# Performance work log

Measured on AMD Instinct MI355X. Metric: run time of the kernel, lower is better.

Reference implementation:

```python
import jax, jax.numpy as jnp
import numpy as np

N_NODES = 100000
N_EDGES = 3200000
D_FEAT = 256
HIDDEN = 16
OUT = 256
EPS = 1e-12  # tf.math.l2_normalize epsilon


def setup_inputs() -> dict:
    key = jax.random.key(0)
    ks = jax.random.split(key, 9)
    x = jax.random.normal(ks[0], (N_NODES, D_FEAT), dtype=jnp.float32)
    src = jax.random.randint(ks[1], (N_EDGES,), 0, N_NODES, dtype=jnp.int32)
    dst = jax.random.randint(ks[2], (N_EDGES,), 0, N_NODES, dtype=jnp.int32)
    s_in = 1.0 / np.sqrt(D_FEAT)
    s_h = 1.0 / np.sqrt(HIDDEN)
    W_node = jax.random.normal(ks[3], (D_FEAT, OUT), dtype=jnp.float32) * s_in
    b_node = jnp.zeros((OUT,), dtype=jnp.float32)
    W_agg = jax.random.normal(ks[4], (D_FEAT, HIDDEN), dtype=jnp.float32) * s_in
    b_agg = jnp.zeros((HIDDEN,), dtype=jnp.float32)
    W_neigh = jax.random.normal(ks[5], (HIDDEN, OUT), dtype=jnp.float32) * s_h
    b_neigh = jnp.zeros((OUT,), dtype=jnp.float32)
    return {"x": x, "src": src, "dst": dst,
            "W_node": W_node, "b_node": b_node,
            "W_agg": W_agg, "b_agg": b_agg,
            "W_neigh": W_neigh, "b_neigh": b_neigh}


def reference(x, src, dst, W_node, b_node, W_agg, b_agg, W_neigh, b_neigh):
    # h = node_layer(x)                       [N, OUT]
    h = x @ W_node + b_node
    # agg features on each node = agg_layer(x) [N, HIDDEN]
    h_agg = x @ W_agg + b_agg
    # message = src node's h_agg; reduce = max over incoming edges per dst
    msgs = h_agg[src]                         # [E, HIDDEN]
    agg = jax.ops.segment_max(msgs, dst, num_segments=N_NODES)  # [N, HIDDEN]
    # nodes with no in-edges: DGL zero-fills; segment_max gives -inf
    agg = jnp.where(jnp.isfinite(agg), agg, 0.0)
    # neighs = neighbour_layer(agg)           [N, OUT]
    neighs = agg @ W_neigh + b_neigh
    new_h = jnp.concatenate([h, neighs], axis=-1)  # [N, 2*OUT]
    # activation is identity (None); l2_normalize along last axis
    sq = jnp.sum(new_h * new_h, axis=-1, keepdims=True)
    return new_h * jax.lax.rsqrt(jnp.maximum(sq, EPS))
```

## Files before the change

### kernel.cpp

```cpp
#include <hip/hip_runtime.h>

#define N_NODES 100000
#define N_EDGES 3200000
#define D_FEAT 256
#define HIDDEN 16
#define OUT 256
#define N_TILES 3125
#define PLANE ((size_t)N_NODES * 8)
#define NBUK 196
#define BSZ 512
#define CAP_G 20480
#define NPLANE 4

typedef __attribute__((ext_vector_type(8))) _Float16 half8;
typedef __attribute__((ext_vector_type(4))) float f32x4;

__device__ __forceinline__ unsigned umax32(unsigned a, unsigned b) { return a > b ? a : b; }
__device__ __forceinline__ unsigned pmax16x2(unsigned a, unsigned b) {
    return umax32(a & 0xFFFFu, b & 0xFFFFu) | (umax32(a >> 16, b >> 16) << 16);
}

__device__ __forceinline__ unsigned short enc16(unsigned short u) {
    return (u & 0x8000) ? (unsigned short)~u : (unsigned short)(u | 0x8000);
}
__device__ __forceinline__ _Float16 dec16(unsigned short e) {
    if (e == 0) return (_Float16)0.f;
    unsigned short b = (e & 0x8000) ? (unsigned short)(e & 0x7FFF) : (unsigned short)~e;
    return __builtin_bit_cast(_Float16, b);
}

__device__ __noinline__ void fb_cas(const unsigned* hpk, unsigned* a4, int sv, int dv) {
    #pragma unroll
    for (int p = 0; p < 8; ++p) {
        unsigned mine = hpk[(size_t)sv * 8 + p];
        unsigned* addr = a4 + (size_t)dv * 8 + p;
        unsigned cur = *addr;
        unsigned nv = pmax16x2(cur, mine);
        while (nv != cur) {
            unsigned old = atomicCAS(addr, cur, nv);
            if (old == cur) break;
            cur = old;
            nv = pmax16x2(cur, mine);
        }
    }
}

__global__ void k_pack(const float* __restrict__ Wn, const float* __restrict__ Wng,
                       const float* __restrict__ Wag,
                       _Float16* __restrict__ Wp, _Float16* __restrict__ Wnp,
                       _Float16* __restrict__ Wap)
{
    int id = blockIdx.x * 256 + threadIdx.x;
    if (id < 8192) {
        int l = id & 63, kb = (id >> 6) & 7, nb = id >> 9;
        int col = nb * 16 + (l & 15);
        int k0 = kb * 32 + (l >> 4) * 8;
        half8 v;
        #pragma unroll
        for (int j = 0; j < 8; ++j) v[j] = (_Float16)Wn[(size_t)(k0 + j) * OUT + col];
        ((half8*)Wp)[id] = v;
    } else if (id < 9216) {
        int id2 = id - 8192;
        int l = id2 & 63, nb = id2 >> 6;
        int col = nb * 16 + (l & 15);
        int k0 = (l >> 4) * 8;
        half8 v;
        #pragma unroll
        for (int j = 0; j < 8; ++j) {
            int k = k0 + j;
            v[j] = (k < HIDDEN) ? (_Float16)Wng[(size_t)k * OUT + col] : (_Float16)0.f;
        }
        ((half8*)Wnp)[id2] = v;
    } else if (id < 9728) {
        int id3 = id - 9216;
        int l = id3 & 63, kb = id3 >> 6;
        int col = l & 15;
        int k0 = kb * 32 + (l >> 4) * 8;
        half8 v;
        #pragma unroll
        for (int j = 0; j < 8; ++j) v[j] = (_Float16)Wag[(size_t)(k0 + j) * HIDDEN + col];
        ((half8*)Wap)[id3] = v;
    }
}

__global__ __launch_bounds__(256) void k_gemm(
    const float* __restrict__ x, const _Float16* __restrict__ Wp,
    const _Float16* __restrict__ Wap, const float* __restrict__ b_node,
    const float* __restrict__ b_agg, unsigned* __restrict__ hpk,
    unsigned* __restrict__ aencP, unsigned* __restrict__ gcnt,
    float* __restrict__ out)
{
    __shared__ _Float16 xs[32][256];
    __shared__ unsigned short eagg[32][18];

    int t = threadIdx.x;
    if (blockIdx.x == 0 && t < NBUK) gcnt[t] = 0u;

    int base = blockIdx.x * 32;

    {
        const float4* xg = (const float4*)(x + (size_t)base * D_FEAT) + (size_t)t * 8;
        float4 v[8];
        #pragma unroll
        for (int i = 0; i < 8; ++i) v[i] = xg[i];
        half8* dst = (half8*)(&xs[t >> 3][(t & 7) * 32]);
        #pragma unroll
        for (int i = 0; i < 4; ++i) {
            float4 u0 = v[2 * i], u1 = v[2 * i + 1];
            half8 h;
            h[0]=(_Float16)u0.x; h[1]=(_Float16)u0.y; h[2]=(_Float16)u0.z; h[3]=(_Float16)u0.w;
            h[4]=(_Float16)u1.x; h[5]=(_Float16)u1.y; h[6]=(_Float16)u1.z; h[7]=(_Float16)u1.w;
            dst[i] = h;
        }
    }
    __syncthreads();

    int w = t >> 6, l = t & 63, lr = l & 15, lg = l >> 4;

    f32x4 acc[2][4];
    #pragma unroll
    for (int mb = 0; mb < 2; ++mb)
        #pragma unroll
        for (int nb = 0; nb < 4; ++nb) acc[mb][nb] = (f32x4){0.f, 0.f, 0.f, 0.f};
    f32x4 agga[2];
    #pragma unroll
    for (int mb = 0; mb < 2; ++mb) agga[mb] = (f32x4){0.f, 0.f, 0.f, 0.f};

    const half8* WpV = (const half8*)Wp;
    const half8* WaV = (const half8*)Wap;

    #pragma unroll
    for (int kb = 0; kb < 8; ++kb) {
        half8 a[2];
        #pragma unroll
        for (int mb = 0; mb < 2; ++mb)
            a[mb] = *(const half8*)(&xs[mb * 16 + lr][kb * 32 + lg * 8]);
        half8 b[4];
        #pragma unroll
        for (int nb = 0; nb < 4; ++nb)
            b[nb] = WpV[((w * 4 + nb) * 8 + kb) * 64 + l];
        if (w == 0) {
            half8 bg = WaV[kb * 64 + l];
            #pragma unroll
            for (int mb = 0; mb < 2; ++mb)
                agga[mb] = __builtin_amdgcn_mfma_f32_16x16x32_f16(a[mb], bg, agga[mb], 0, 0, 0);
        }
        #pragma unroll
        for (int mb = 0; mb < 2; ++mb)
            #pragma unroll
            for (int nb = 0; nb < 4; ++nb)
                acc[mb][nb] = __builtin_amdgcn_mfma_f32_16x16x32_f16(
                    a[mb], b[nb], acc[mb][nb], 0, 0, 0);
    }

    if (w == 0) {
        float ba = b_agg[lr];
        #pragma unroll
        for (int mb = 0; mb < 2; ++mb)
            #pragma unroll
            for (int r = 0; r < 4; ++r) {
                float val = agga[mb][r] + ba;
                eagg[mb * 16 + lg * 4 + r][lr] =
                    enc16(__builtin_bit_cast(unsigned short, (_Float16)val));
            }
    }
    __syncthreads();

    {
        int node = t >> 3, p = t & 7;
        int gn = base + node;
        unsigned lo = eagg[node][2 * p], hi = eagg[node][2 * p + 1];
        unsigned word = lo | (hi << 16);
        size_t idx = (size_t)gn * 8 + p;
        hpk[idx] = word;
        aencP[(size_t)NPLANE * PLANE + idx] = 0u;
    }

    float bnc[4];
    #pragma unroll
    for (int nb = 0; nb < 4; ++nb) bnc[nb] = b_node[w * 64 + nb * 16 + lr];
    half8 hv8[4];
    #pragma unroll
    for (int mb = 0; mb < 2; ++mb)
        #pragma unroll
        for (int nb = 0; nb < 4; ++nb)
            #pragma unroll
            for (int r = 0; r < 4; ++r) {
                int idx = mb * 16 + nb * 4 + r;
                hv8[idx >> 3][idx & 7] = (_Float16)(acc[mb][nb][r] + bnc[nb]);
            }
    char* hb = (char*)out + (size_t)(base + (t >> 3)) * 2048 + 1024 + (size_t)(t & 7) * 64;
    #pragma unroll
    for (int i = 0; i < 4; ++i)
        ((half8*)hb)[i] = hv8[i];
}

__global__ __launch_bounds__(256) void k_bin(
    const int* __restrict__ src, const int* __restrict__ dst,
    const unsigned* __restrict__ hpk,
    unsigned* __restrict__ gbin, unsigned* __restrict__ gcnt,
    unsigned* __restrict__ a4)
{
    __shared__ unsigned lbuf[NBUK * 64];
    __shared__ unsigned lcnt[NBUK];
    __shared__ unsigned gbase[NBUK];
    int t = threadIdx.x;
    for (int i = t; i < NBUK; i += 256) lcnt[i] = 0u;
    __syncthreads();

    int start = blockIdx.x * 4000;
    #pragma unroll 4
    for (int it = 0; it < 16; ++it) {
        int j = it * 256 + t;
        if (j < 4000) {
            int idx = start + j;
            int sv = src[idx], dv = dst[idx];
            int bk = dv >> 9;
            unsigned ev = ((unsigned)sv << 9) | (unsigned)(dv & 511);
            unsigned r = atomicAdd(&lcnt[bk], 1u);
            if (r < 64) lbuf[bk * 64 + r] = ev;
            else fb_cas(hpk, a4, sv, dv);
        }
    }
    __syncthreads();

    if (t < NBUK) {
        unsigned c = lcnt[t]; if (c > 64) c = 64;
        gbase[t] = atomicAdd(&gcnt[t], c);
    }
    __syncthreads();

    int wv = t >> 6, ln = t & 63;
    for (int b = wv; b < NBUK; b += 4) {
        unsigned c = lcnt[b]; if (c > 64) c = 64;
        if (ln < (int)c) {
            unsigned pos = gbase[b] + (unsigned)ln;
            unsigned ev = lbuf[b * 64 + ln];
            if (pos < CAP_G) gbin[(size_t)b * CAP_G + pos] = ev;
            else fb_cas(hpk, a4, (int)(ev >> 9), b * BSZ + (int)(ev & 511));
        }
    }
}

__global__ __launch_bounds__(256) void k_bucket(
    const unsigned* __restrict__ gbin, const unsigned* __restrict__ gcnt,
    const unsigned* __restrict__ hpk, unsigned* __restrict__ aencP)
{
    __shared__ unsigned tab[BSZ * 17];
    int t = threadIdx.x;
    int b = blockIdx.x % NBUK;
    int k = blockIdx.x / NBUK;
    for (int i = t; i < BSZ * 17; i += 256) tab[i] = 0u;
    __syncthreads();

    int cnt = (int)gcnt[b]; if (cnt > CAP_G) cnt = CAP_G;
    int s = (cnt * k) >> 2;
    int e = (cnt * (k + 1)) >> 2;
    int p = t & 7;
    const unsigned* gb = gbin + (size_t)b * CAP_G;

    int i = s + (t >> 3);
    for (; i + 96 < e; i += 128) {
        unsigned ev0 = gb[i], ev1 = gb[i + 32], ev2 = gb[i + 64], ev3 = gb[i + 96];
        unsigned p0 = hpk[(size_t)(ev0 >> 9) * 8 + p];
        unsigned p1 = hpk[(size_t)(ev1 >> 9) * 8 + p];
        unsigned p2 = hpk[(size_t)(ev2 >> 9) * 8 + p];
        unsigned p3 = hpk[(size_t)(ev3 >> 9) * 8 + p];
        {
            int a0 = (int)(ev0 & 511) * 17 + 2 * p;
            unsigned lo = p0 & 0xFFFFu, hi = p0 >> 16;
            if (lo > tab[a0])     atomicMax(&tab[a0], lo);
            if (hi > tab[a0 + 1]) atomicMax(&tab[a0 + 1], hi);
        }
        {
            int a1 = (int)(ev1 & 511) * 17 + 2 * p;
            unsigned lo = p1 & 0xFFFFu, hi = p1 >> 16;
            if (lo > tab[a1])     atomicMax(&tab[a1], lo);
            if (hi > tab[a1 + 1]) atomicMax(&tab[a1 + 1], hi);
        }
        {
            int a2 = (int)(ev2 & 511) * 17 + 2 * p;
            unsigned lo = p2 & 0xFFFFu, hi = p2 >> 16;
            if (lo > tab[a2])     atomicMax(&tab[a2], lo);
            if (hi > tab[a2 + 1]) atomicMax(&tab[a2 + 1], hi);
        }
        {
            int a3 = (int)(ev3 & 511) * 17 + 2 * p;
            unsigned lo = p3 & 0xFFFFu, hi = p3 >> 16;
            if (lo > tab[a3])     atomicMax(&tab[a3], lo);
            if (hi > tab[a3 + 1]) atomicMax(&tab[a3 + 1], hi);
        }
    }
    for (; i < e; i += 32) {
        unsigned ev = gb[i];
        unsigned pair = hpk[(size_t)(ev >> 9) * 8 + p];
        int a0 = (int)(ev & 511) * 17 + 2 * p;
        unsigned lo = pair & 0xFFFFu, hi = pair >> 16;
        if (lo > tab[a0])     atomicMax(&tab[a0], lo);
        if (hi > tab[a0 + 1]) atomicMax(&tab[a0 + 1], hi);
    }
    __syncthreads();

    for (int j = t; j < BSZ * 8; j += 256) {
        int n = j >> 3, pp = j & 7;
        int gn = b * BSZ + n;
        if (gn < N_NODES) {
            unsigned wd = tab[n * 17 + 2 * pp] | (tab[n * 17 + 2 * pp + 1] << 16);
            aencP[(size_t)k * PLANE + (size_t)gn * 8 + pp] = wd;
        }
    }
}

__global__ __launch_bounds__(256) void k_epi(
    const unsigned* __restrict__ aencP, const _Float16* __restrict__ Wnp,
    const float* __restrict__ b_neigh, float* __restrict__ out)
{
    __shared__ _Float16 aggL[32][40];
    __shared__ float ss[4][32];
    __shared__ float invl[32];

    int t = threadIdx.x;
    int w = t >> 6, l = t & 63, lr = l & 15, lg = l >> 4;
    int base = blockIdx.x * 32;

    {
        int nl = t >> 3, p = t & 7;
        int gn = base + nl;
        size_t idx = (size_t)gn * 8 + p;
        unsigned v = 0u;
        #pragma unroll
        for (int k5 = 0; k5 <= NPLANE; ++k5)
            v = pmax16x2(v, aencP[(size_t)k5 * PLANE + idx]);
        aggL[nl][2 * p]     = dec16((unsigned short)(v & 0xFFFFu));
        aggL[nl][2 * p + 1] = dec16((unsigned short)(v >> 16));
    }
    for (int i = t; i < 32 * 16; i += 256)
        aggL[i >> 4][16 + (i & 15)] = (_Float16)0.f;

    const char* hb = (const char*)out + (size_t)(base + (t >> 3)) * 2048 + 1024 + (size_t)(t & 7) * 64;
    half8 hv8[4];
    #pragma unroll
    for (int i = 0; i < 4; ++i)
        hv8[i] = ((const half8*)hb)[i];

    __syncthreads();

    f32x4 nacc[2][4];
    {
        half8 an[2], bn[4];
        #pragma unroll
        for (int mb = 0; mb < 2; ++mb)
            an[mb] = *(const half8*)(&aggL[mb * 16 + lr][lg * 8]);
        #pragma unroll
        for (int nb = 0; nb < 4; ++nb)
            bn[nb] = ((const half8*)Wnp)[(w * 4 + nb) * 64 + l];
        f32x4 z = (f32x4){0.f, 0.f, 0.f, 0.f};
        #pragma unroll
        for (int mb = 0; mb < 2; ++mb)
            #pragma unroll
            for (int nb = 0; nb < 4; ++nb)
                nacc[mb][nb] = __builtin_amdgcn_mfma_f32_16x16x32_f16(
                    an[mb], bn[nb], z, 0, 0, 0);
    }

    float bec[4];
    #pragma unroll
    for (int nb = 0; nb < 4; ++nb) bec[nb] = b_neigh[w * 64 + nb * 16 + lr];
    #pragma unroll
    for (int mb = 0; mb < 2; ++mb)
        #pragma unroll
        for (int nb = 0; nb < 4; ++nb)
            #pragma unroll
            for (int r = 0; r < 4; ++r)
                nacc[mb][nb][r] += bec[nb];

    #pragma unroll
    for (int mb = 0; mb < 2; ++mb) {
        float p[4] = {0.f, 0.f, 0.f, 0.f};
        #pragma unroll
        for (int nb = 0; nb < 4; ++nb)
            #pragma unroll
            for (int r = 0; r < 4; ++r) {
                int idx = mb * 16 + nb * 4 + r;
                float hf = (float)hv8[idx >> 3][idx & 7];
                p[r] += hf * hf + nacc[mb][nb][r] * nacc[mb][nb][r];
            }
        #pragma unroll
        for (int r = 0; r < 4; ++r) {
            float v = p[r];
            v += __shfl_xor(v, 1);
            v += __shfl_xor(v, 2);
            v += __shfl_xor(v, 4);
            v += __shfl_xor(v, 8);
            if (lr == 0) ss[w][mb * 16 + lg * 4 + r] = v;
        }
    }
    __syncthreads();
    if (t < 32) {
        float sq = ss[0][t] + ss[1][t] + ss[2][t] + ss[3][t];
        invl[t] = rsqrtf(fmaxf(sq, 1e-12f));
    }
    __syncthreads();

    #pragma unroll
    for (int mb = 0; mb < 2; ++mb)
        #pragma unroll
        for (int r = 0; r < 4; ++r) {
            int slot = mb * 16 + lg * 4 + r;
            int node = base + slot;
            float inv = invl[slot];
            size_t row = (size_t)node * (2 * OUT);
            #pragma unroll
            for (int nb = 0; nb < 4; ++nb) {
                int col = w * 64 + nb * 16 + lr;
                int idx = mb * 16 + nb * 4 + r;
                out[row + col] = (float)hv8[idx >> 3][idx & 7] * inv;
                out[row + OUT + col] = nacc[mb][nb][r] * inv;
            }
        }
}

extern "C" void kernel_launch(void* const* d_in, const int* in_sizes, int n_in,
                              void* d_out, int out_size, void* d_ws, size_t ws_size,
                              hipStream_t stream) {
    const float* x       = (const float*)d_in[0];
    const int*   src     = (const int*)d_in[1];
    const int*   dst     = (const int*)d_in[2];
    const float* W_node  = (const float*)d_in[3];
    const float* b_node  = (const float*)d_in[4];
    const float* W_agg   = (const float*)d_in[5];
    const float* b_agg   = (const float*)d_in[6];
    const float* W_neigh = (const float*)d_in[7];
    const float* b_neigh = (const float*)d_in[8];
    float* out = (float*)d_out;

    char* ws = (char*)d_ws;
    unsigned*  hpk   = (unsigned*)ws;      ws += (size_t)N_NODES * 8 * 4;
    unsigned*  aencP = (unsigned*)ws;      ws += (size_t)(NPLANE + 1) * PLANE * 4;
    unsigned*  gbin  = (unsigned*)ws;      ws += (size_t)NBUK * CAP_G * 4;
    unsigned*  gcnt  = (unsigned*)ws;      ws += 1024;
    _Float16*  Wp    = (_Float16*)ws;      ws += (size_t)16 * 8 * 64 * 8 * 2;
    _Float16*  Wnp   = (_Float16*)ws;      ws += (size_t)16 * 64 * 8 * 2;
    _Float16*  Wap   = (_Float16*)ws;

    unsigned* a4 = aencP + (size_t)NPLANE * PLANE;

    k_pack<<<38, 256, 0, stream>>>(W_node, W_neigh, W_agg, Wp, Wnp, Wap);

    k_gemm<<<N_TILES, 256, 0, stream>>>(x, Wp, Wap, b_node, b_agg,
                                        hpk, aencP, gcnt, out);

    k_bin<<<800, 256, 0, stream>>>(src, dst, hpk, gbin, gcnt, a4);

    k_bucket<<<NBUK * NPLANE, 256, 0, stream>>>(gbin, gcnt, hpk, aencP);

    k_epi<<<N_TILES, 256, 0, stream>>>(aencP, Wnp, b_neigh, out);
}
```

Measured before the change: 189.5 us.

## Process two node tiles per GEMM block with prefetch of the second tile

Each k_gemm block now handles two 32-node tiles. The second tile's x rows are loaded into registers before computing the first, then converted to fp16 into a second shared buffer after the first tile's MFMA loop. The aim is to hide global-load latency behind compute and to reuse the weight fragments across tiles via cache. In exchange it halves the grid, raises register pressure (v1 holds 32 floats) and doubles LDS per block, which may lower occupancy.

```diff
diff --git a/kernel.cpp b/kernel.cpp
--- a/kernel.cpp
+++ b/kernel.cpp
@@ -90,20 +90,25 @@
     unsigned* __restrict__ aencP, unsigned* __restrict__ gcnt,
     float* __restrict__ out)
 {
-    __shared__ _Float16 xs[32][256];
+    __shared__ _Float16 xs[2][32][256];
     __shared__ unsigned short eagg[32][18];
 
     int t = threadIdx.x;
     if (blockIdx.x == 0 && t < NBUK) gcnt[t] = 0u;
 
-    int base = blockIdx.x * 32;
+    int w = t >> 6, l = t & 63, lr = l & 15, lg = l >> 4;
+    int tile0 = blockIdx.x * 2;
+    bool has1 = (tile0 + 1 < N_TILES);
+
+    const half8* WpV = (const half8*)Wp;
+    const half8* WaV = (const half8*)Wap;
 
     {
-        const float4* xg = (const float4*)(x + (size_t)base * D_FEAT) + (size_t)t * 8;
+        const float4* xg = (const float4*)(x + (size_t)tile0 * 32 * D_FEAT) + (size_t)t * 8;
         float4 v[8];
         #pragma unroll
         for (int i = 0; i < 8; ++i) v[i] = xg[i];
-        half8* dst = (half8*)(&xs[t >> 3][(t & 7) * 32]);
+        half8* dst = (half8*)(&xs[0][t >> 3][(t & 7) * 32]);
         #pragma unroll
         for (int i = 0; i < 4; ++i) {
             float4 u0 = v[2 * i], u1 = v[2 * i + 1];
@@ -113,86 +118,107 @@
             dst[i] = h;
         }
     }
-    __syncthreads();
-
-    int w = t >> 6, l = t & 63, lr = l & 15, lg = l >> 4;
-
-    f32x4 acc[2][4];
-    #pragma unroll
-    for (int mb = 0; mb < 2; ++mb)
-        #pragma unroll
-        for (int nb = 0; nb < 4; ++nb) acc[mb][nb] = (f32x4){0.f, 0.f, 0.f, 0.f};
-    f32x4 agga[2];
-    #pragma unroll
-    for (int mb = 0; mb < 2; ++mb) agga[mb] = (f32x4){0.f, 0.f, 0.f, 0.f};
-
-    const half8* WpV = (const half8*)Wp;
-    const half8* WaV = (const half8*)Wap;
-
-    #pragma unroll
-    for (int kb = 0; kb < 8; ++kb) {
-        half8 a[2];
+    float4 v1[8];
+    if (has1) {
+        const float4* xg = (const float4*)(x + (size_t)(tile0 + 1) * 32 * D_FEAT) + (size_t)t * 8;
+        #pragma unroll
+        for (int i = 0; i < 8; ++i) v1[i] = xg[i];
+    }
+    __syncthreads();
+
+    #pragma unroll 1
+    for (int ph = 0; ph < 2; ++ph) {
+        if (ph == 1 && !has1) break;
+        int base = (tile0 + ph) * 32;
+
+        f32x4 acc[2][4];
         #pragma unroll
         for (int mb = 0; mb < 2; ++mb)
-            a[mb] = *(const half8*)(&xs[mb * 16 + lr][kb * 32 + lg * 8]);
-        half8 b[4];
-        #pragma unroll
-        for (int nb = 0; nb < 4; ++nb)
-            b[nb] = WpV[((w * 4 + nb) * 8 + kb) * 64 + l];
+            #pragma unroll
+            for (int nb = 0; nb < 4; ++nb) acc[mb][nb] = (f32x4){0.f, 0.f, 0.f, 0.f};
+        f32x4 agga[2];
+        #pragma unroll
+        for (int mb = 0; mb < 2; ++mb) agga[mb] = (f32x4){0.f, 0.f, 0.f, 0.f};
+
+        #pragma unroll
+        for (int kb = 0; kb < 8; ++kb) {
+            half8 a[2];
+            #pragma unroll
+            for (int mb = 0; mb < 2; ++mb)
+                a[mb] = *(const half8*)(&xs[ph][mb * 16 + lr][kb * 32 + lg * 8]);
+            half8 b[4];
+            #pragma unroll
+            for (int nb = 0; nb < 4; ++nb)
+                b[nb] = WpV[((w * 4 + nb) * 8 + kb) * 64 + l];
+            if (w == 0) {
+                half8 bg = WaV[kb * 64 + l];
+                #pragma unroll
+                for (int mb = 0; mb < 2; ++mb)
+                    agga[mb] = __builtin_amdgcn_mfma_f32_16x16x32_f16(a[mb], bg, agga[mb], 0, 0, 0);
+            }
+            #pragma unroll
+            for (int mb = 0; mb < 2; ++mb)
+                #pragma unroll
+                for (int nb = 0; nb < 4; ++nb)
+                    acc[mb][nb] = __builtin_amdgcn_mfma_f32_16x16x32_f16(
+                        a[mb], b[nb], acc[mb][nb], 0, 0, 0);
+        }
+
+        if (ph == 0 && has1) {
+            half8* dst = (half8*)(&xs[1][t >> 3][(t & 7) * 32]);
+            #pragma unroll
+            for (int i = 0; i < 4; ++i) {
+                float4 u0 = v1[2 * i], u1 = v1[2 * i + 1];
+                half8 h;
+                h[0]=(_Float16)u0.x; h[1]=(_Float16)u0.y; h[2]=(_Float16)u0.z; h[3]=(_Float16)u0.w;
+                h[4]=(_Float16)u1.x; h[5]=(_Float16)u1.y; h[6]=(_Float16)u1.z; h[7]=(_Float16)u1.w;
+                dst[i] = h;
+            }
+        }
+
         if (w == 0) {
-            half8 bg = WaV[kb * 64 + l];
+            float ba = b_agg[lr];
             #pragma unroll
             for (int mb = 0; mb < 2; ++mb)
-                agga[mb] = __builtin_amdgcn_mfma_f32_16x16x32_f16(a[mb], bg, agga[mb], 0, 0, 0);
-        }
+                #pragma unroll
+                for (int r = 0; r < 4; ++r) {
+                    float val = agga[mb][r] + ba;
+                    eagg[mb * 16 + lg * 4 + r][lr] =
+                        enc16(__builtin_bit_cast(unsigned short, (_Float16)val));
+                }
+        }
+        __syncthreads();
+
+        {
+            int node = t >> 3, p = t & 7;
+            int gn = base + node;
+            unsigned lo = eagg[node][2 * p], hi = eagg[node][2 * p + 1];
+            unsigned word = lo | (hi << 16);
+            size_t idx = (size_t)gn * 8 + p;
+            hpk[idx] = word;
+            aencP[(size_t)NPLANE * PLANE + idx] = 0u;
+        }
+
+        float bnc[4];
+        #pragma unroll
+        for (int nb = 0; nb < 4; ++nb) bnc[nb] = b_node[w * 64 + nb * 16 + lr];
+        half8 hv8[4];
         #pragma unroll
         for (int mb = 0; mb < 2; ++mb)
             #pragma unroll
             for (int nb = 0; nb < 4; ++nb)
-                acc[mb][nb] = __builtin_amdgcn_mfma_f32_16x16x32_f16(
-                    a[mb], b[nb], acc[mb][nb], 0, 0, 0);
-    }
-
-    if (w == 0) {
-        float ba = b_agg[lr];
-        #pragma unroll
-        for (int mb = 0; mb < 2; ++mb)
-            #pragma unroll
-            for (int r = 0; r < 4; ++r) {
-                float val = agga[mb][r] + ba;
-                eagg[mb * 16 + lg * 4 + r][lr] =
-                    enc16(__builtin_bit_cast(unsigned short, (_Float16)val));
-            }
-    }
-    __syncthreads();
-
-    {
-        int node = t >> 3, p = t & 7;
-        int gn = base + node;
-        unsigned lo = eagg[node][2 * p], hi = eagg[node][2 * p + 1];
-        unsigned word = lo | (hi << 16);
-        size_t idx = (size_t)gn * 8 + p;
-        hpk[idx] = word;
-        aencP[(size_t)NPLANE * PLANE + idx] = 0u;
-    }
-
-    float bnc[4];
-    #pragma unroll
-    for (int nb = 0; nb < 4; ++nb) bnc[nb] = b_node[w * 64 + nb * 16 + lr];
-    half8 hv8[4];
-    #pragma unroll
-    for (int mb = 0; mb < 2; ++mb)
-        #pragma unroll
-        for (int nb = 0; nb < 4; ++nb)
-            #pragma unroll
-            for (int r = 0; r < 4; ++r) {
-                int idx = mb * 16 + nb * 4 + r;
-                hv8[idx >> 3][idx & 7] = (_Float16)(acc[mb][nb][r] + bnc[nb]);
-            }
-    char* hb = (char*)out + (size_t)(base + (t >> 3)) * 2048 + 1024 + (size_t)(t & 7) * 64;
-    #pragma unroll
-    for (int i = 0; i < 4; ++i)
-        ((half8*)hb)[i] = hv8[i];
+                #pragma unroll
+                for (int r = 0; r < 4; ++r) {
+                    int idx = mb * 16 + nb * 4 + r;
+                    hv8[idx >> 3][idx & 7] = (_Float16)(acc[mb][nb][r] + bnc[nb]);
+                }
+        char* hb = (char*)out + (size_t)(base + (t >> 3)) * 2048 + 1024 + (size_t)(t & 7) * 64;
+        #pragma unroll
+        for (int i = 0; i < 4; ++i)
+            ((half8*)hb)[i] = hv8[i];
+
+        if (ph == 0) __syncthreads();
+    }
 }
 
 __global__ __launch_bounds__(256) void k_bin(
@@ -447,8 +473,8 @@
 
     k_pack<<<38, 256, 0, stream>>>(W_node, W_neigh, W_agg, Wp, Wnp, Wap);
 
-    k_gemm<<<N_TILES, 256, 0, stream>>>(x, Wp, Wap, b_node, b_agg,
-                                        hpk, aencP, gcnt, out);
+    k_gemm<<<(N_TILES + 1) / 2, 256, 0, stream>>>(x, Wp, Wap, b_node, b_agg,
+                                                  hpk, aencP, gcnt, out);
 
     k_bin<<<800, 256, 0, stream>>>(src, dst, hpk, gbin, gcnt, a4);
 
```

After: 224.9 us. 1.19x slower.
